# Kernel tuning notes

Measured on AMD Instinct MI355X. Metric: run time of the kernel, lower is better.

## Reference

```python
import jax, jax.numpy as jnp
import numpy as np

TAU = 0.01
RHO = 1.99
SIGMA = 1.0 / TAU / 72.0  # 1/tau/72 as in __init__
N_IT = 10  # n_it_max


def nabla2(x):
    # forward finite differences: channel 0 along W (last axis), channel 1 along H
    u = jnp.zeros(x.shape + (2,), x.dtype)
    u = u.at[..., :, :-1, 0].add(x[..., :, 1:] - x[..., :, :-1])
    u = u.at[..., :-1, :, 1].add(x[..., 1:, :] - x[..., :-1, :])
    return u


def nabla2_adjoint(u):
    x = jnp.zeros(u.shape[:-1], u.dtype)
    x = x.at[..., :, :-1].add(-u[..., :, :-1, 0])
    x = x.at[..., :, 1:].add(u[..., :, :-1, 0])
    x = x.at[..., :-1, :].add(-u[..., :-1, :, 1])
    x = x.at[..., 1:, :].add(u[..., :-1, :, 1])
    return x


def epsilon2(I):
    # Jacobian of the vector field I [..., H, W, 2] -> G [..., H, W, 4]
    I0, I1 = I[..., 0], I[..., 1]
    G = jnp.zeros(I0.shape + (4,), I.dtype)
    G = G.at[..., 0].add(I0)                                  # G0 = I0 - shift_H(I0)
    G = G.at[..., 1:, :, 0].add(-I0[..., :-1, :])
    G = G.at[..., :, 1:, 1].add(I0[..., :, 1:] - I0[..., :, :-1])  # G1: W-diff of I0
    G = G.at[..., 2].add(I1)                                  # G2 = I1 - shift_W(I1)
    G = G.at[..., :, 1:, 2].add(-I1[..., :, :-1])
    G = G.at[..., :-1, :, 3].add(I1[..., 1:, :] - I1[..., :-1, :])  # G3: H-diff of I1
    return G


def epsilon2_adjoint(G):
    I = jnp.zeros(G.shape[:-1] + (2,), G.dtype)
    I = I.at[..., 0].add(G[..., 0])
    I = I.at[..., :-1, :, 0].add(-G[..., 1:, :, 0])
    I = I.at[..., :, :-1, 0].add(-G[..., :, 1:, 1])
    I = I.at[..., :, 1:, 0].add(G[..., :, 1:, 1])
    I = I.at[..., 1].add(G[..., 2])
    I = I.at[..., :, :-1, 1].add(-G[..., :, 1:, 2])
    I = I.at[..., :-1, :, 1].add(-G[..., :-1, :, 3])
    I = I.at[..., 1:, :, 1].add(G[..., :-1, :, 3])
    return I


def setup_inputs() -> dict:
    key = jax.random.key(0)
    y = jax.random.normal(key, (4, 512, 512), dtype=jnp.float32)
    return {"y": y, "ths": 1}


def reference(y, ths):
    lam1 = ths * 0.1
    lam2 = ths * 0.15

    def prox_tau_fr(r):
        left = jnp.sqrt(jnp.sum(r * r, axis=-1)) / (TAU * lam1)
        return r - r / jnp.maximum(left, 1.0)[..., None]

    def prox_sigma_g_conj(u):
        return u / jnp.maximum(jnp.sqrt(jnp.sum(u * u, axis=-1)) / lam2, 1.0)[..., None]

    x2 = y
    r2 = jnp.zeros(y.shape + (2,), y.dtype)
    u2 = jnp.zeros(y.shape + (4,), y.dtype)

    def step(carry, _):
        x2, r2, u2 = carry
        tmp = TAU * epsilon2_adjoint(u2)
        x = (x2 - nabla2_adjoint(tmp) + TAU * y) / (1.0 + TAU)  # prox_tau_fx
        r = prox_tau_fr(r2 + tmp)
        u = prox_sigma_g_conj(
            u2 + SIGMA * epsilon2(nabla2(2.0 * x - x2) - (2.0 * r - r2))
        )
        x2 = x2 + RHO * (x - x2)
        r2 = r2 + RHO * (r - r2)
        u2 = u2 + RHO * (u - u2)
        return (x2, r2, u2), None

    (x2, r2, u2), _ = jax.lax.scan(step, (x2, r2, u2), None, length=N_IT)
    return x2
```

## Files before the change

kernel.cpp:

```cpp
#include <hip/hip_runtime.h>
#include <hip/hip_fp16.h>
#include <math.h>

#define HH 512
#define WW 512
#define BB 4
#define NPIX (BB * HH * WW)

#define HS 4
#define NSX 9
#define NBAND (HH / HS)
#define NWAVES (NSX * NBAND * BB)
#define NBLK (NWAVES / 4)

constexpr float TAUf   = 0.01f;
constexpr float RHOf   = 1.99f;
constexpr float SIGMAf = (float)(1.0 / 0.01 / 72.0);
constexpr float INV1PT = (float)(1.0 / 1.01);

__device__ __forceinline__ float SD(float v) { return __shfl_down(v, 1, 64); }
__device__ __forceinline__ unsigned SDu(unsigned v) { return __shfl_down(v, 1, 64); }
__device__ __forceinline__ float SUp(float v) { return __shfl_up(v, 1, 64); }


template <int MODE>
__global__ __launch_bounds__(256) void sweep(
    const float* __restrict__ y, const int* __restrict__ ths_p,
    const uint2* __restrict__ f_in, const uint2* __restrict__ u_in,
    uint2* __restrict__ f_out, uint2* __restrict__ u_out,
    float* __restrict__ xout)
{
    const int tid  = threadIdx.x;
    const int lane = tid & 63;
    const int wid  = blockIdx.x * 4 + (tid >> 6);
    const int sx   = wid % NSX;
    const int t2   = wid / NSX;
    const int band = t2 & (NBAND - 1);
    const int b    = t2 / NBAND;
    const int R0   = band * HS;
    const int w    = sx * 60 - 2 + lane;
    const int boff = b * (HH * WW);
    const bool wok = ((unsigned)w) < (unsigned)WW;
    const float mA = (w >= 1 && w < WW) ? 1.f : 0.f;
    const float mB = (w >= 0 && w < WW - 1) ? 1.f : 0.f;
    const bool cok = (lane >= 2) && (lane < 62) && (w < WW);

    const float ths  = (float)ths_p[0];
    const float tl1_ = TAUf * (ths * 0.1f);
    const float l2_  = ths * 0.15f;

    float uf0[4], uf1[4], uf2[4], uf3[4];
    unsigned u12r[4];
    float i0r[2], i1r[2];
    float sr[2];
    float t1r[2];
    float v0r[4];
    float v1r[2];
    #pragma unroll
    for (int q = 0; q < 4; ++q) { uf0[q]=uf1[q]=uf2[q]=uf3[q]=0.f; v0r[q]=0.f; u12r[q]=0u; }
    i0r[0]=i0r[1]=i1r[0]=i1r[1]=0.f;
    sr[0]=sr[1]=0.f; t1r[0]=t1r[1]=0.f; v1r[0]=v1r[1]=0.f;

    auto uload = [&](int row) -> uint2 {
        uint2 z; z.x = 0u; z.y = 0u;
        if (((unsigned)row) < (unsigned)HH && wok)
            z = u_in[(size_t)(boff + row * WW + w)];
        return z;
    };
    auto fload = [&](int row) -> uint2 {
        uint2 z; z.x = 0u; z.y = 0u;
        if (((unsigned)row) < (unsigned)HH && wok)
            z = f_in[(size_t)(boff + row * WW + w)];
        return z;
    };
    auto unpk = [&](int slot, uint2 raw) {
        __half2 lo = *(reinterpret_cast<__half2*>(&raw.x));
        __half2 hi = *(reinterpret_cast<__half2*>(&raw.y));
        uf0[slot] = __low2float(lo); uf1[slot] = __high2float(lo);
        uf2[slot] = __low2float(hi); uf3[slot] = __high2float(hi);
        u12r[slot] = (raw.x >> 16) | (raw.y << 16);
    };
    auto compI = [&](int rr, int islot, int c, int d, int uu_) {
        if (((unsigned)rr) < (unsigned)HH) {
            float hD  = (rr < HH - 1) ? 1.f : 0.f;
            unsigned pp = SDu(u12r[c]);
            __half2 ph = *(reinterpret_cast<__half2*>(&pp));
            float u1n = __low2float(ph);
            float u2n = __high2float(ph);
            i0r[islot] = uf0[c] - uf0[d] - u1n + mA * uf1[c];
            i1r[islot] = uf2[c] - u2n - hD * uf3[c] + uf3[uu_];
        } else { i0r[islot] = 0.f; i1r[islot] = 0.f; }
    };

    if (MODE == 2) {
        unpk(2, uload(R0 - 2));
        unpk(3, uload(R0 - 1));
        unpk(0, uload(R0));
        compI(R0 - 1, 1, 3, 0, 2);
        uint2 puA = uload(R0 + 1);
        uint2 puB = uload(R0 + 2);
        uint2 pfA = fload(R0);
        uint2 pfB = fload(R0 + 1);
        #pragma unroll
        for (int k = 0; k < HS; ++k) {
            const int rr = R0 + k;
            unpk((k + 1) & 3, puA);
            puA = puB;
            if (k < HS - 2) puB = uload(R0 + k + 3);
            __half2 lo = *(reinterpret_cast<__half2*>(&pfA.x));
            __half2 hi = *(reinterpret_cast<__half2*>(&pfA.y));
            float x2v = __low2float(lo);
            float yv  = __high2float(hi);
            pfA = pfB;
            if (k < HS - 2) pfB = fload(R0 + k + 2);
            compI(rr, k & 1, k & 3, (k + 1) & 3, (k + 3) & 3);
            float hD = (rr < HH - 1) ? 1.f : 0.f;
            float i0c = i0r[k & 1], i1c = i1r[k & 1], i1u = i1r[(k + 1) & 1];
            float i0l = SUp(i0c);
            float na = TAUf * (mA * i0l - mB * i0c + i1u - hD * i1c);
            float x = (x2v - na + TAUf * yv) * INV1PT;
            if (cok) xout[boff + rr * WW + w] = x2v + RHOf * (x - x2v);
        }
        return;
    }

    auto compS = [&](int rr, int isc, int isp,
                     float yv, float x2v, float r20v, float r21v, unsigned yraw,
                     bool coreRow, float &sOut, float &t0Out, float &t1Out) {
        if (((unsigned)rr) < (unsigned)HH) {
            if (MODE == 0) {
                sOut = yv; t0Out = 0.f; t1Out = 0.f;
                if (coreRow && cok) {
                    int idx = boff + rr * WW + w;
                    unsigned hb = (unsigned)__half_as_ushort(__float2half(yv));
                    uint2 st; st.x = hb; st.y = hb << 16;
                    f_out[(size_t)idx] = st;
                }
            } else {
                float hD = (rr < HH - 1) ? 1.f : 0.f;
                float i0c = i0r[isc], i1c = i1r[isc], i1u = i1r[isp];
                float i0l = SUp(i0c);
                float na = TAUf * (mA * i0l - mB * i0c + i1u - hD * i1c);
                float x = (x2v - na + TAUf * yv) * INV1PT;
                float rr0 = r20v + TAUf * i0c;
                float rr1 = r21v + TAUf * i1c;
                float d = rr0 * rr0 + rr1 * rr1;
                float rinv = fminf(tl1_ * __builtin_amdgcn_rsqf(d), 1.0f);
                float r0 = rr0 - rr0 * rinv;
                float r1 = rr1 - rr1 * rinv;
                sOut  = 2.f * x  - x2v;
                t0Out = 2.f * r0 - r20v;
                t1Out = 2.f * r1 - r21v;
                if (coreRow && cok) {
                    int idx = boff + rr * WW + w;
                    __half2 lo2 = __floats2half2_rn(x2v + RHOf * (x - x2v),
                                                    r20v + RHOf * (r0 - r20v));
                    unsigned r1b = (unsigned)__half_as_ushort(
                        __float2half(r21v + RHOf * (r1 - r21v)));
                    uint2 st; st.x = *(unsigned*)&lo2; st.y = r1b | (yraw << 16);
                    f_out[(size_t)idx] = st;
                }
            }
        } else { sOut = 0.f; t0Out = 0.f; t1Out = 0.f; }
    };

    auto compU = [&](int ro, int v0c_s, int v0u_s, int v1c_s, int v1d_s, int uslot) {
        float hD  = (ro < HH - 1) ? 1.f : 0.f;
        float v0c = v0r[v0c_s], v0u = v0r[v0u_s];
        float v1c = v1r[v1c_s], v1d = v1r[v1d_s];
        float v0l = SUp(v0c);
        float v1l = SUp(v1c);
        float G0 = v0c - v0u;
        float G1 = mA * (v0c - v0l);
        float G2 = v1c - mA * v1l;
        float G3 = hD * (v1d - v1c);
        float u0v, u1v, u2v, u3v;
        if (MODE == 0) { u0v = u1v = u2v = u3v = 0.f; }
        else { u0v = uf0[uslot]; u1v = uf1[uslot]; u2v = uf2[uslot]; u3v = uf3[uslot]; }
        float uu0 = u0v + SIGMAf * G0;
        float uu1 = u1v + SIGMAf * G1;
        float uu2 = u2v + SIGMAf * G2;
        float uu3 = u3v + SIGMAf * G3;
        float d = uu0 * uu0 + uu1 * uu1 + uu2 * uu2 + uu3 * uu3;
        float ui = fminf(l2_ * __builtin_amdgcn_rsqf(d), 1.0f);
        if (cok) {
            int idx = boff + ro * WW + w;
            __half2 lo = __floats2half2_rn(u0v + RHOf * (uu0 * ui - u0v),
                                           u1v + RHOf * (uu1 * ui - u1v));
            __half2 hi = __floats2half2_rn(u2v + RHOf * (uu2 * ui - u2v),
                                           u3v + RHOf * (uu3 * ui - u3v));
            uint2 st; st.x = *(unsigned*)&lo; st.y = *(unsigned*)&hi;
            u_out[(size_t)idx] = st;
        }
    };

    uint2 puA, puB, pfA, pfB;
    puA.x = puA.y = puB.x = puB.y = 0u;
    pfA.x = pfA.y = pfB.x = pfB.y = 0u;
    float pyA = 0.f, pyB = 0.f;
    if (MODE != 0) {
        unpk(1, uload(R0 - 3));
        unpk(2, uload(R0 - 2));
        unpk(3, uload(R0 - 1));
        compI(R0 - 2, 0, 2, 3, 1);
        puA = uload(R0);
        puB = uload(R0 + 1);
        pfA = fload(R0 - 1);
        pfB = fload(R0);
    } else {
        int rowA = R0 - 1; bool okA = (((unsigned)rowA) < (unsigned)HH) && wok;
        pyA = okA ? y[boff + rowA * WW + w] : 0.f;
        pyB = wok ? y[boff + R0 * WW + w] : 0.f;
    }

    #pragma unroll
    for (int k = 0; k < HS + 3; ++k) {
        const int rr = R0 - 1 + k;

        float yv, x2v = 0.f, r20v = 0.f, r21v = 0.f; unsigned yraw = 0u;
        if (MODE != 0) {
            unpk(k & 3, puA);
            puA = puB;
            if (k <= HS) puB = uload(R0 + k + 2);
            __half2 lo = *(reinterpret_cast<__half2*>(&pfA.x));
            __half2 hi = *(reinterpret_cast<__half2*>(&pfA.y));
            x2v  = __low2float(lo);  r20v = __high2float(lo);
            r21v = __low2float(hi);  yv   = __high2float(hi);
            yraw = pfA.y >> 16;
            pfA = pfB;
            if (k <= HS) pfB = fload(R0 + k + 1);
        } else {
            yv = pyA;
            pyA = pyB;
            if (k <= HS) {
                int row = R0 + k + 1;
                bool ok = (((unsigned)row) < (unsigned)HH) && wok;
                pyB = ok ? y[boff + row * WW + w] : 0.f;
            }
        }
        if (MODE != 0) compI(rr, (k + 1) & 1, (k + 3) & 3, k & 3, (k + 2) & 3);

        float sN, t0N, t1N;
        compS(rr, (k + 1) & 1, k & 1, yv, x2v, r20v, r21v, yraw,
              (k >= 1 && k <= HS), sN, t0N, t1N);

        {
            float sPrev  = sr[k & 1];
            float t1Prev = t1r[k & 1];
            float hDm1   = (rr < HH) ? 1.f : 0.f;
            v0r[(k + 3) & 3] = mB * (SD(sN) - sN) - t0N;
            v1r[k & 1]       = hDm1 * (sN - sPrev) - t1Prev;
            sr[(k + 1) & 1]  = sN;
            t1r[(k + 1) & 1] = t1N;
        }

        if (k >= 3) compU(R0 - 3 + k, (k + 1) & 3, k & 3, (k + 1) & 1, k & 1,
                          (k + 1) & 3);
    }
}

extern "C" void kernel_launch(void* const* d_in, const int* in_sizes, int n_in,
                              void* d_out, int out_size, void* d_ws, size_t ws_size,
                              hipStream_t stream)
{
    const float* y   = (const float*)d_in[0];
    const int*   ths = (const int*)d_in[1];
    uint2* ws2 = (uint2*)d_ws;

    uint2* FA = ws2;
    uint2* UA = ws2 + (size_t)NPIX;
    uint2* FB = ws2 + 2 * (size_t)NPIX;
    uint2* UB = ws2 + 3 * (size_t)NPIX;
    float* xout = (float*)d_out;

    dim3 block(256);
    dim3 grid(NBLK);

    sweep<0><<<grid, block, 0, stream>>>(y, ths, nullptr, nullptr, FB, UB, nullptr);
    uint2 *fi = FB, *ui = UB, *fo = FA, *uo = UA;
    for (int it = 1; it <= 8; ++it) {
        sweep<1><<<grid, block, 0, stream>>>(y, ths, fi, ui, fo, uo, nullptr);
        uint2* t;
        t = fi; fi = fo; fo = t;
        t = ui; ui = uo; uo = t;
    }
    sweep<2><<<grid, block, 0, stream>>>(y, ths, fi, ui, nullptr, nullptr, xout);
}
```

Measured before the change: 161.2 us.

## Fuse first two primal-dual iterations into one kernel reading y directly

Adds a fused01 kernel that computes iteration 0 (from y, with zero r and u) and iteration 1 together in one row sweep. The iteration-0 u values are kept in registers rather than written to memory and read back. The column strip shrinks from 60 to 58 output pixels per wave to widen the halo for the extra stencil depth. This removes one launch and one full read/write pass over the workspace, at the cost of some redundant halo compute. MODE 0 of sweep is deleted as dead code.

```diff
diff --git a/kernel.cpp b/kernel.cpp
--- a/kernel.cpp
+++ b/kernel.cpp
@@ -52,10 +52,8 @@
     float uf0[4], uf1[4], uf2[4], uf3[4];
     unsigned u12r[4];
     float i0r[2], i1r[2];
-    float sr[2];
-    float t1r[2];
-    float v0r[4];
-    float v1r[2];
+    float sr[2], t1r[2];
+    float v0r[4], v1r[2];
     #pragma unroll
     for (int q = 0; q < 4; ++q) { uf0[q]=uf1[q]=uf2[q]=uf3[q]=0.f; v0r[q]=0.f; u12r[q]=0u; }
     i0r[0]=i0r[1]=i1r[0]=i1r[1]=0.f;
@@ -128,38 +126,28 @@
                      float yv, float x2v, float r20v, float r21v, unsigned yraw,
                      bool coreRow, float &sOut, float &t0Out, float &t1Out) {
         if (((unsigned)rr) < (unsigned)HH) {
-            if (MODE == 0) {
-                sOut = yv; t0Out = 0.f; t1Out = 0.f;
-                if (coreRow && cok) {
-                    int idx = boff + rr * WW + w;
-                    unsigned hb = (unsigned)__half_as_ushort(__float2half(yv));
-                    uint2 st; st.x = hb; st.y = hb << 16;
-                    f_out[(size_t)idx] = st;
-                }
-            } else {
-                float hD = (rr < HH - 1) ? 1.f : 0.f;
-                float i0c = i0r[isc], i1c = i1r[isc], i1u = i1r[isp];
-                float i0l = SUp(i0c);
-                float na = TAUf * (mA * i0l - mB * i0c + i1u - hD * i1c);
-                float x = (x2v - na + TAUf * yv) * INV1PT;
-                float rr0 = r20v + TAUf * i0c;
-                float rr1 = r21v + TAUf * i1c;
-                float d = rr0 * rr0 + rr1 * rr1;
-                float rinv = fminf(tl1_ * __builtin_amdgcn_rsqf(d), 1.0f);
-                float r0 = rr0 - rr0 * rinv;
-                float r1 = rr1 - rr1 * rinv;
-                sOut  = 2.f * x  - x2v;
-                t0Out = 2.f * r0 - r20v;
-                t1Out = 2.f * r1 - r21v;
-                if (coreRow && cok) {
-                    int idx = boff + rr * WW + w;
-                    __half2 lo2 = __floats2half2_rn(x2v + RHOf * (x - x2v),
-                                                    r20v + RHOf * (r0 - r20v));
-                    unsigned r1b = (unsigned)__half_as_ushort(
-                        __float2half(r21v + RHOf * (r1 - r21v)));
-                    uint2 st; st.x = *(unsigned*)&lo2; st.y = r1b | (yraw << 16);
-                    f_out[(size_t)idx] = st;
-                }
+            float hD = (rr < HH - 1) ? 1.f : 0.f;
+            float i0c = i0r[isc], i1c = i1r[isc], i1u = i1r[isp];
+            float i0l = SUp(i0c);
+            float na = TAUf * (mA * i0l - mB * i0c + i1u - hD * i1c);
+            float x = (x2v - na + TAUf * yv) * INV1PT;
+            float rr0 = r20v + TAUf * i0c;
+            float rr1 = r21v + TAUf * i1c;
+            float d = rr0 * rr0 + rr1 * rr1;
+            float rinv = fminf(tl1_ * __builtin_amdgcn_rsqf(d), 1.0f);
+            float r0 = rr0 - rr0 * rinv;
+            float r1 = rr1 - rr1 * rinv;
+            sOut  = 2.f * x  - x2v;
+            t0Out = 2.f * r0 - r20v;
+            t1Out = 2.f * r1 - r21v;
+            if (coreRow && cok) {
+                int idx = boff + rr * WW + w;
+                __half2 lo2 = __floats2half2_rn(x2v + RHOf * (x - x2v),
+                                                r20v + RHOf * (r0 - r20v));
+                unsigned r1b = (unsigned)__half_as_ushort(
+                    __float2half(r21v + RHOf * (r1 - r21v)));
+                uint2 st; st.x = *(unsigned*)&lo2; st.y = r1b | (yraw << 16);
+                f_out[(size_t)idx] = st;
             }
         } else { sOut = 0.f; t0Out = 0.f; t1Out = 0.f; }
     };
@@ -174,9 +162,7 @@
         float G1 = mA * (v0c - v0l);
         float G2 = v1c - mA * v1l;
         float G3 = hD * (v1d - v1c);
-        float u0v, u1v, u2v, u3v;
-        if (MODE == 0) { u0v = u1v = u2v = u3v = 0.f; }
-        else { u0v = uf0[uslot]; u1v = uf1[uslot]; u2v = uf2[uslot]; u3v = uf3[uslot]; }
+        float u0v = uf0[uslot], u1v = uf1[uslot], u2v = uf2[uslot], u3v = uf3[uslot];
         float uu0 = u0v + SIGMAf * G0;
         float uu1 = u1v + SIGMAf * G1;
         float uu2 = u2v + SIGMAf * G2;
@@ -197,48 +183,32 @@
     uint2 puA, puB, pfA, pfB;
     puA.x = puA.y = puB.x = puB.y = 0u;
     pfA.x = pfA.y = pfB.x = pfB.y = 0u;
-    float pyA = 0.f, pyB = 0.f;
-    if (MODE != 0) {
-        unpk(1, uload(R0 - 3));
-        unpk(2, uload(R0 - 2));
-        unpk(3, uload(R0 - 1));
-        compI(R0 - 2, 0, 2, 3, 1);
-        puA = uload(R0);
-        puB = uload(R0 + 1);
-        pfA = fload(R0 - 1);
-        pfB = fload(R0);
-    } else {
-        int rowA = R0 - 1; bool okA = (((unsigned)rowA) < (unsigned)HH) && wok;
-        pyA = okA ? y[boff + rowA * WW + w] : 0.f;
-        pyB = wok ? y[boff + R0 * WW + w] : 0.f;
-    }
+    unpk(1, uload(R0 - 3));
+    unpk(2, uload(R0 - 2));
+    unpk(3, uload(R0 - 1));
+    compI(R0 - 2, 0, 2, 3, 1);
+    puA = uload(R0);
+    puB = uload(R0 + 1);
+    pfA = fload(R0 - 1);
+    pfB = fload(R0);
 
     #pragma unroll
     for (int k = 0; k < HS + 3; ++k) {
         const int rr = R0 - 1 + k;
-
-        float yv, x2v = 0.f, r20v = 0.f, r21v = 0.f; unsigned yraw = 0u;
-        if (MODE != 0) {
-            unpk(k & 3, puA);
-            puA = puB;
-            if (k <= HS) puB = uload(R0 + k + 2);
-            __half2 lo = *(reinterpret_cast<__half2*>(&pfA.x));
-            __half2 hi = *(reinterpret_cast<__half2*>(&pfA.y));
-            x2v  = __low2float(lo);  r20v = __high2float(lo);
-            r21v = __low2float(hi);  yv   = __high2float(hi);
-            yraw = pfA.y >> 16;
-            pfA = pfB;
-            if (k <= HS) pfB = fload(R0 + k + 1);
-        } else {
-            yv = pyA;
-            pyA = pyB;
-            if (k <= HS) {
-                int row = R0 + k + 1;
-                bool ok = (((unsigned)row) < (unsigned)HH) && wok;
-                pyB = ok ? y[boff + row * WW + w] : 0.f;
-            }
-        }
-        if (MODE != 0) compI(rr, (k + 1) & 1, (k + 3) & 3, k & 3, (k + 2) & 3);
+        unpk(k & 3, puA);
+        puA = puB;
+        if (k <= HS) puB = uload(R0 + k + 2);
+        __half2 lo = *(reinterpret_cast<__half2*>(&pfA.x));
+        __half2 hi = *(reinterpret_cast<__half2*>(&pfA.y));
+        float x2v  = __low2float(lo);
+        float r20v = __high2float(lo);
+        float r21v = __low2float(hi);
+        float yv   = __high2float(hi);
+        unsigned yraw = pfA.y >> 16;
+        pfA = pfB;
+        if (k <= HS) pfB = fload(R0 + k + 1);
+
+        compI(rr, (k + 1) & 1, (k + 3) & 3, k & 3, (k + 2) & 3);
 
         float sN, t0N, t1N;
         compS(rr, (k + 1) & 1, k & 1, yv, x2v, r20v, r21v, yraw,
@@ -259,6 +229,187 @@
     }
 }
 
+__global__ __launch_bounds__(256) void fused01(
+    const float* __restrict__ y, const int* __restrict__ ths_p,
+    uint2* __restrict__ f_out, uint2* __restrict__ u_out)
+{
+    const int tid  = threadIdx.x;
+    const int lane = tid & 63;
+    const int wid  = blockIdx.x * 4 + (tid >> 6);
+    const int sx   = wid % NSX;
+    const int t2   = wid / NSX;
+    const int band = t2 & (NBAND - 1);
+    const int b    = t2 / NBAND;
+    const int R0   = band * HS;
+    const int w    = sx * 58 - 3 + lane;
+    const int boff = b * (HH * WW);
+    const bool wok = ((unsigned)w) < (unsigned)WW;
+    const float mA = (w >= 1 && w < WW) ? 1.f : 0.f;
+    const float mB = (w >= 0 && w < WW - 1) ? 1.f : 0.f;
+    const bool cok = (lane >= 3) && (lane <= 60) && (w < WW);
+
+    const float ths  = (float)ths_p[0];
+    const float tl1_ = TAUf * (ths * 0.1f);
+    const float l2_  = ths * 0.15f;
+
+    float p0r[4];
+    float p1r[2];
+    float yD1 = 0.f, yD2 = 0.f, yD3 = 0.f;
+
+    float uf0[4], uf1[4], uf2[4], uf3[4];
+    unsigned u12r[4];
+    float i0r[2], i1r[2];
+    float sr[2], t1r[2];
+    float v0r[4], v1r[2];
+    #pragma unroll
+    for (int q = 0; q < 4; ++q) {
+        uf0[q]=uf1[q]=uf2[q]=uf3[q]=0.f; v0r[q]=0.f; u12r[q]=0u; p0r[q]=0.f;
+    }
+    i0r[0]=i0r[1]=i1r[0]=i1r[1]=0.f;
+    sr[0]=sr[1]=0.f; t1r[0]=t1r[1]=0.f; v1r[0]=v1r[1]=0.f; p1r[0]=p1r[1]=0.f;
+
+    auto yload = [&](int row) -> float {
+        return (((unsigned)row) < (unsigned)HH && wok)
+                   ? y[boff + row * WW + w] : 0.f;
+    };
+    auto unpk = [&](int slot, uint2 raw) {
+        __half2 lo = *(reinterpret_cast<__half2*>(&raw.x));
+        __half2 hi = *(reinterpret_cast<__half2*>(&raw.y));
+        uf0[slot] = __low2float(lo); uf1[slot] = __high2float(lo);
+        uf2[slot] = __low2float(hi); uf3[slot] = __high2float(hi);
+        u12r[slot] = (raw.x >> 16) | (raw.y << 16);
+    };
+    auto compI = [&](int rr, int islot, int c, int d, int uu_) {
+        if (((unsigned)rr) < (unsigned)HH) {
+            float hD  = (rr < HH - 1) ? 1.f : 0.f;
+            unsigned pp = SDu(u12r[c]);
+            __half2 ph = *(reinterpret_cast<__half2*>(&pp));
+            float u1n = __low2float(ph);
+            float u2n = __high2float(ph);
+            i0r[islot] = uf0[c] - uf0[d] - u1n + mA * uf1[c];
+            i1r[islot] = uf2[c] - u2n - hD * uf3[c] + uf3[uu_];
+        } else { i0r[islot] = 0.f; i1r[islot] = 0.f; }
+    };
+
+    float pyA = yload(R0 - 4);
+    float pyB = yload(R0 - 3);
+
+    #pragma unroll
+    for (int j = 0; j < HS + 9; ++j) {
+        const int p = R0 - 4 + j;
+        float yp = pyA; pyA = pyB;
+        if (j <= HS + 6) pyB = yload(R0 - 2 + j);
+
+        p0r[j & 3]       = mB * (SD(yp) - yp);
+        p1r[(j + 1) & 1] = ((p < HH) ? 1.f : 0.f) * (yp - yD1);
+
+        if (j >= 3) {
+            const int ro = R0 - 6 + j;
+            float hD  = (ro < HH - 1) ? 1.f : 0.f;
+            float v0c = p0r[(j + 2) & 3], v0u = p0r[(j + 1) & 3];
+            float v1c = p1r[j & 1],       v1d = p1r[(j + 1) & 1];
+            float G0 = v0c - v0u;
+            float G1 = mA * (v0c - SUp(v0c));
+            float G2 = v1c - mA * SUp(v1c);
+            float G3 = hD * (v1d - v1c);
+            float uu0 = SIGMAf * G0, uu1 = SIGMAf * G1;
+            float uu2 = SIGMAf * G2, uu3 = SIGMAf * G3;
+            float d = uu0*uu0 + uu1*uu1 + uu2*uu2 + uu3*uu3;
+            float ui = fminf(l2_ * __builtin_amdgcn_rsqf(d), 1.0f);
+            __half2 lo = __floats2half2_rn(RHOf * (uu0 * ui), RHOf * (uu1 * ui));
+            __half2 hi = __floats2half2_rn(RHOf * (uu2 * ui), RHOf * (uu3 * ui));
+            uint2 st; st.x = *(unsigned*)&lo; st.y = *(unsigned*)&hi;
+            unpk((j + 2) & 3, st);
+        }
+
+        if (j == 5) compI(R0 - 2, 0, 2, 3, 1);
+
+        if (j >= 6) {
+            const int k  = j - 6;
+            const int rr = R0 - 1 + k;
+            __half yh = __float2half(yD3);
+            float yv  = __half2float(yh);
+            unsigned yraw = (unsigned)__half_as_ushort(yh);
+
+            compI(rr, (k + 1) & 1, (k + 3) & 3, k & 3, (k + 2) & 3);
+
+            float sN, t0N, t1N;
+            {
+                const bool coreRow = (k >= 1 && k <= HS);
+                if (((unsigned)rr) < (unsigned)HH) {
+                    float hD = (rr < HH - 1) ? 1.f : 0.f;
+                    float i0c = i0r[(k + 1) & 1], i1c = i1r[(k + 1) & 1];
+                    float i1u = i1r[k & 1];
+                    float i0l = SUp(i0c);
+                    float na = TAUf * (mA * i0l - mB * i0c + i1u - hD * i1c);
+                    float x = (yv - na + TAUf * yv) * INV1PT;
+                    float rr0 = TAUf * i0c;
+                    float rr1 = TAUf * i1c;
+                    float d2 = rr0*rr0 + rr1*rr1;
+                    float rinv = fminf(tl1_ * __builtin_amdgcn_rsqf(d2), 1.0f);
+                    float r0 = rr0 - rr0 * rinv;
+                    float r1 = rr1 - rr1 * rinv;
+                    sN  = 2.f * x - yv;
+                    t0N = 2.f * r0;
+                    t1N = 2.f * r1;
+                    if (coreRow && cok) {
+                        int idx = boff + rr * WW + w;
+                        __half2 lo2 = __floats2half2_rn(yv + RHOf * (x - yv),
+                                                        RHOf * r0);
+                        unsigned r1b = (unsigned)__half_as_ushort(
+                            __float2half(RHOf * r1));
+                        uint2 st2; st2.x = *(unsigned*)&lo2;
+                        st2.y = r1b | (yraw << 16);
+                        f_out[(size_t)idx] = st2;
+                    }
+                } else { sN = 0.f; t0N = 0.f; t1N = 0.f; }
+            }
+
+            {
+                float sPrev  = sr[k & 1];
+                float t1Prev = t1r[k & 1];
+                float hDm1   = (rr < HH) ? 1.f : 0.f;
+                v0r[(k + 3) & 3] = mB * (SD(sN) - sN) - t0N;
+                v1r[k & 1]       = hDm1 * (sN - sPrev) - t1Prev;
+                sr[(k + 1) & 1]  = sN;
+                t1r[(k + 1) & 1] = t1N;
+            }
+
+            if (k >= 3) {
+                const int ro = R0 - 3 + k;
+                float hD  = (ro < HH - 1) ? 1.f : 0.f;
+                float v0c = v0r[(k + 1) & 3], v0u = v0r[k & 3];
+                float v1c = v1r[(k + 1) & 1], v1d = v1r[k & 1];
+                float v0l = SUp(v0c);
+                float v1l = SUp(v1c);
+                float G0 = v0c - v0u;
+                float G1 = mA * (v0c - v0l);
+                float G2 = v1c - mA * v1l;
+                float G3 = hD * (v1d - v1c);
+                const int us = (k + 1) & 3;
+                float u0v = uf0[us], u1v = uf1[us], u2v = uf2[us], u3v = uf3[us];
+                float uu0 = u0v + SIGMAf * G0;
+                float uu1 = u1v + SIGMAf * G1;
+                float uu2 = u2v + SIGMAf * G2;
+                float uu3 = u3v + SIGMAf * G3;
+                float d = uu0*uu0 + uu1*uu1 + uu2*uu2 + uu3*uu3;
+                float ui = fminf(l2_ * __builtin_amdgcn_rsqf(d), 1.0f);
+                if (cok) {
+                    int idx = boff + ro * WW + w;
+                    __half2 lo = __floats2half2_rn(u0v + RHOf * (uu0 * ui - u0v),
+                                                   u1v + RHOf * (uu1 * ui - u1v));
+                    __half2 hi = __floats2half2_rn(u2v + RHOf * (uu2 * ui - u2v),
+                                                   u3v + RHOf * (uu3 * ui - u3v));
+                    uint2 st; st.x = *(unsigned*)&lo; st.y = *(unsigned*)&hi;
+                    u_out[(size_t)idx] = st;
+                }
+            }
+        }
+
+        yD3 = yD2; yD2 = yD1; yD1 = yp;
+    }
+}
+
 extern "C" void kernel_launch(void* const* d_in, const int* in_sizes, int n_in,
                               void* d_out, int out_size, void* d_ws, size_t ws_size,
                               hipStream_t stream)
@@ -276,9 +427,9 @@
     dim3 block(256);
     dim3 grid(NBLK);
 
-    sweep<0><<<grid, block, 0, stream>>>(y, ths, nullptr, nullptr, FB, UB, nullptr);
-    uint2 *fi = FB, *ui = UB, *fo = FA, *uo = UA;
-    for (int it = 1; it <= 8; ++it) {
+    fused01<<<grid, block, 0, stream>>>(y, ths, FA, UA);
+    uint2 *fi = FA, *ui = UA, *fo = FB, *uo = UB;
+    for (int it = 2; it <= 8; ++it) {
         sweep<1><<<grid, block, 0, stream>>>(y, ths, fi, ui, fo, uo, nullptr);
         uint2* t;
         t = fi; fi = fo; fo = t;
```

Result: faster. 155.8 us (-3.3%).
